# Performance work log

Hardware: AMD Instinct MI355X
Metric: run time of the kernel (lower is better)

Reference implementation:

```python
import jax, jax.numpy as jnp
import numpy as np

DISCARD_RATIOS = [0.25, 1.0, 1.0, 1.0, 0.25, 0.25, 1.0, 1.0, 1.0, 1.0, 0.25, 0.25]
START_LAYER = 4
SKIP_LAYERS = {5, 6, 7, 8, 9, 10}

L, B, H, N = 12, 32, 12, 197


def setup_inputs() -> dict:
    key = jax.random.key(0)
    # post-softmax-like attention weights: positive, uniform in [0,1)
    attentions = jax.random.uniform(key, (L, B, H, N, N), dtype=jnp.float32)
    return {"attentions": attentions}


def reference(attentions) -> jnp.ndarray:
    Ln, Bn, Hn, Nn, _ = attentions.shape
    I = jnp.eye(Nn, dtype=attentions.dtype)            # [N,N]
    result = jnp.broadcast_to(I, (Bn, Nn, Nn))         # [B,N,N]
    b_idx = jnp.arange(Bn)[:, None]                    # [B,1] for batched scatter
    for layer in range(START_LAYER, Ln):
        if layer in SKIP_LAYERS:
            continue
        attn = attentions[layer].mean(axis=1)          # head fusion 'mean' -> [B,N,N]
        k = int(Nn * Nn * DISCARD_RATIOS[layer])       # static per-layer discard count
        if k > 0:
            flat = attn.reshape(Bn, -1)                # [B, N*N]
            # indices of the k SMALLEST entries per batch (torch topk largest=False)
            _, idx = jax.lax.top_k(-flat, k)           # [B,k]
            col0 = flat[:, 0]                          # protect flat index 0 (CLS->CLS)
            flat = flat.at[b_idx, idx].set(0.0)
            flat = flat.at[:, 0].set(col0)
            attn = flat.reshape(Bn, Nn, Nn)
        attn = (attn + I[None]) * 0.5
        attn = attn / attn.sum(axis=-1, keepdims=True)
        result = jnp.einsum('bij,bjk->bik', attn, result)
    return result


if __name__ == "__main__":
    out = reference(**setup_inputs())
    print(out.shape, out.dtype)
```

## Files before the change

### kernel.cpp

```cpp
#include <hip/hip_runtime.h>
#include <stdint.h>

#define Lc   12
#define Bc   32
#define Hc   12
#define Nc   197
#define NNc  (Nc * Nc)
#define Kc   9702
#define NLB  64

#define HBINS 2048
#define CAP   2048

__global__ void __launch_bounds__(256) head_mean_kernel(const float* __restrict__ in,
                                                        float* __restrict__ mean) {
    int j  = blockIdx.x * 256 + threadIdx.x;
    int lb = blockIdx.y;
    if (j >= NNc) return;
    int lsel  = lb >> 5;
    int b     = lb & 31;
    int layer = lsel ? 11 : 4;
    const float* base = in + ((size_t)(layer * Bc + b)) * Hc * NNc + j;
    float acc = 0.0f;
    #pragma unroll
    for (int h = 0; h < Hc; ++h) acc += base[(size_t)h * NNc];
    mean[(size_t)lb * NNc + j] = acc / 12.0f;
}

__global__ void __launch_bounds__(256) select_kernel(const float* __restrict__ mean,
                                                     int* __restrict__ thr_out,
                                                     int* __restrict__ cut_out) {
    const int lb  = blockIdx.x;
    const int tid = threadIdx.x;
    const float* v = mean + (size_t)lb * NNc;

    __shared__ int hist[HBINS];
    __shared__ int chunk[256];
    __shared__ int s_bin, s_cum, s_cnt;
    __shared__ int list[CAP];

    const int shifts[3] = {21, 10, 0};
    const int masks[3]  = {0x7FF, 0x7FF, 0x3FF};

    int kreq = Kc;
    unsigned prefix = 0;

    for (int pass = 0; pass < 3; ++pass) {
        for (int i = tid; i < HBINS; i += 256) hist[i] = 0;
        __syncthreads();
        for (int i = tid; i < NNc; i += 256) {
            unsigned bits = __float_as_uint(v[i]);
            bool ok = (pass == 0) || ((bits >> shifts[pass - 1]) == prefix);
            if (ok) atomicAdd(&hist[(bits >> shifts[pass]) & masks[pass]], 1);
        }
        __syncthreads();
        int s = 0;
        #pragma unroll
        for (int q = 0; q < 8; ++q) s += hist[tid * 8 + q];
        chunk[tid] = s;
        __syncthreads();
        if (tid == 0) {
            int run = 0;
            for (int t = 0; t < 256; ++t) { int tmp = chunk[t]; chunk[t] = run; run += tmp; }
        }
        __syncthreads();
        {
            int c = chunk[tid];
            #pragma unroll
            for (int q = 0; q < 8; ++q) {
                int h = hist[tid * 8 + q];
                if (c < kreq && c + h >= kreq) { s_bin = tid * 8 + q; s_cum = c; }
                c += h;
            }
        }
        __syncthreads();
        kreq -= s_cum;
        if (pass == 0)      prefix = (unsigned)s_bin;
        else if (pass == 1) prefix = (prefix << 11) | (unsigned)s_bin;
        else                prefix = (prefix << 10) | (unsigned)s_bin;
        __syncthreads();
    }

    if (tid == 0) s_cnt = 0;
    __syncthreads();
    for (int i = tid; i < NNc; i += 256) {
        if (__float_as_uint(v[i]) == prefix) {
            int p = atomicAdd(&s_cnt, 1);
            if (p < CAP) list[p] = i;
        }
    }
    __syncthreads();
    if (tid == 0) {
        int m = s_cnt < CAP ? s_cnt : CAP;
        int t = kreq;
        int last = -1;
        for (int s2 = 0; s2 < t && s2 < m; ++s2) {
            int mn = 0x7FFFFFFF;
            for (int q = 0; q < m; ++q) { int x = list[q]; if (x > last && x < mn) mn = x; }
            last = mn;
        }
        thr_out[lb] = (int)prefix;
        cut_out[lb] = last;
    }
}

__global__ void __launch_bounds__(256) norm_kernel(float* __restrict__ buf,
                                                   const int* __restrict__ thr_arr,
                                                   const int* __restrict__ cut_arr) {
    int row = blockIdx.x;
    int lb  = row / Nc;
    int i   = row - lb * Nc;
    float thr  = __uint_as_float((unsigned)thr_arr[lb]);
    int cutoff = cut_arr[lb];
    float* rowp = buf + (size_t)lb * NNc + (size_t)i * Nc;

    int j = threadIdx.x;
    float a = 0.0f;
    if (j < Nc) {
        float vv = rowp[j];
        int idx  = i * Nc + j;
        bool zero = (idx != 0) && (vv < thr || (vv == thr && idx <= cutoff));
        float x = zero ? 0.0f : vv;
        a = (x + (i == j ? 1.0f : 0.0f)) * 0.5f;
    }
    float s = a;
    #pragma unroll
    for (int off = 32; off > 0; off >>= 1) s += __shfl_down(s, off, 64);
    __shared__ float red[4];
    __shared__ float s_tot;
    int wid = threadIdx.x >> 6;
    if ((threadIdx.x & 63) == 0) red[wid] = s;
    __syncthreads();
    if (threadIdx.x == 0) s_tot = red[0] + red[1] + red[2] + red[3];
    __syncthreads();
    if (j < Nc) rowp[j] = a / s_tot;
}

__global__ void __launch_bounds__(256) matmul_kernel(const float* __restrict__ buf,
                                                     float* __restrict__ C) {
    int b  = blockIdx.z;
    const float* A  = buf + (size_t)(32 + b) * NNc;
    const float* Bm = buf + (size_t)b * NNc;
    float* Cb = C + (size_t)b * NNc;

    __shared__ float As[16][17];
    __shared__ float Bs[16][17];
    int tx = threadIdx.x, ty = threadIdx.y;
    int i0 = blockIdx.y * 16, j0 = blockIdx.x * 16;
    float acc = 0.0f;
    for (int k0 = 0; k0 < Nc; k0 += 16) {
        int ar = i0 + ty, ac = k0 + tx;
        As[ty][tx] = (ar < Nc && ac < Nc) ? A[ar * Nc + ac] : 0.0f;
        int br = k0 + ty, bc = j0 + tx;
        Bs[ty][tx] = (br < Nc && bc < Nc) ? Bm[br * Nc + bc] : 0.0f;
        __syncthreads();
        #pragma unroll
        for (int kk = 0; kk < 16; ++kk) acc += As[ty][kk] * Bs[kk][tx];
        __syncthreads();
    }
    int i = i0 + ty, j = j0 + tx;
    if (i < Nc && j < Nc) Cb[i * Nc + j] = acc;
}

extern "C" void kernel_launch(void* const* d_in, const int* in_sizes, int n_in,
                              void* d_out, int out_size, void* d_ws, size_t ws_size,
                              hipStream_t stream) {
    const float* attn = (const float*)d_in[0];
    float* out = (float*)d_out;

    float* buf = (float*)d_ws;
    int*   thr = (int*)((char*)d_ws + (size_t)NLB * NNc * sizeof(float));
    int*   cut = thr + NLB;

    dim3 g1((NNc + 255) / 256, NLB);
    head_mean_kernel<<<g1, 256, 0, stream>>>(attn, buf);

    select_kernel<<<NLB, 256, 0, stream>>>(buf, thr, cut);

    norm_kernel<<<NLB * Nc, 256, 0, stream>>>(buf, thr, cut);

    matmul_kernel<<<dim3(13, 13, Bc), dim3(16, 16), 0, stream>>>(buf, out);
}
```

Before: 928.7 us.

## Vectorize head mean, fuse select with normalization, enlarge matmul tiles

The head-mean kernel now handles four elements per thread into a padded, float4-aligned buffer. The radix-select and row-normalization kernels are merged into a single 1024-thread block per batch-layer, with a wave-level scan replacing the serial prefix sum and float4 loads in the histogram passes. The matmul moves to 32x32 tiles with a 2x2 register block per thread. The fused kernel still runs only 64 blocks, so normalization gets less parallelism than the old per-row launch in exchange for removing a launch and a global round trip.

```diff
diff --git a/kernel.cpp b/kernel.cpp
--- a/kernel.cpp
+++ b/kernel.cpp
@@ -6,74 +6,108 @@
 #define Hc   12
 #define Nc   197
 #define NNc  (Nc * Nc)
+#define NG4  9703
+#define STRIDEc 38812
 #define Kc   9702
 #define NLB  64
 
 #define HBINS 2048
 #define CAP   2048
+#define PADV  2.0f
 
 __global__ void __launch_bounds__(256) head_mean_kernel(const float* __restrict__ in,
                                                         float* __restrict__ mean) {
-    int j  = blockIdx.x * 256 + threadIdx.x;
+    int j4 = blockIdx.x * 256 + threadIdx.x;
     int lb = blockIdx.y;
-    if (j >= NNc) return;
-    int lsel  = lb >> 5;
+    if (j4 >= NG4) return;
     int b     = lb & 31;
-    int layer = lsel ? 11 : 4;
+    int layer = (lb >> 5) ? 11 : 4;
+    int j = j4 * 4;
     const float* base = in + ((size_t)(layer * Bc + b)) * Hc * NNc + j;
-    float acc = 0.0f;
-    #pragma unroll
-    for (int h = 0; h < Hc; ++h) acc += base[(size_t)h * NNc];
-    mean[(size_t)lb * NNc + j] = acc / 12.0f;
-}
-
-__global__ void __launch_bounds__(256) select_kernel(const float* __restrict__ mean,
-                                                     int* __restrict__ thr_out,
-                                                     int* __restrict__ cut_out) {
-    const int lb  = blockIdx.x;
-    const int tid = threadIdx.x;
-    const float* v = mean + (size_t)lb * NNc;
+    float* mp = mean + (size_t)lb * STRIDEc;
+
+    if (j + 4 <= NNc) {
+        float a0 = 0.f, a1 = 0.f, a2 = 0.f, a3 = 0.f;
+        #pragma unroll
+        for (int h = 0; h < Hc; ++h) {
+            const float* p = base + (size_t)h * NNc;
+            a0 += p[0]; a1 += p[1]; a2 += p[2]; a3 += p[3];
+        }
+        float4 r;
+        r.x = a0 / 12.0f; r.y = a1 / 12.0f; r.z = a2 / 12.0f; r.w = a3 / 12.0f;
+        *reinterpret_cast<float4*>(mp + j) = r;
+    } else {
+        for (int e = j; e < STRIDEc; ++e) {
+            if (e < NNc) {
+                float a = 0.f;
+                #pragma unroll
+                for (int h = 0; h < Hc; ++h) a += base[(size_t)h * NNc + (e - j)];
+                mp[e] = a / 12.0f;
+            } else {
+                mp[e] = PADV;
+            }
+        }
+    }
+}
+
+__global__ void __launch_bounds__(1024) select_norm_kernel(float* __restrict__ mean) {
+    const int lb   = blockIdx.x;
+    const int tid  = threadIdx.x;
+    const int lane = tid & 63;
+    const int wid  = tid >> 6;
+    float* vbuf = mean + (size_t)lb * STRIDEc;
+    const float4* v4 = reinterpret_cast<const float4*>(vbuf);
 
     __shared__ int hist[HBINS];
-    __shared__ int chunk[256];
-    __shared__ int s_bin, s_cum, s_cnt;
+    __shared__ int wtot[16];
+    __shared__ int s_bin, s_cum, s_cnt, s_cut;
     __shared__ int list[CAP];
-
-    const int shifts[3] = {21, 10, 0};
-    const int masks[3]  = {0x7FF, 0x7FF, 0x3FF};
 
     int kreq = Kc;
     unsigned prefix = 0;
 
+    #pragma unroll
     for (int pass = 0; pass < 3; ++pass) {
-        for (int i = tid; i < HBINS; i += 256) hist[i] = 0;
-        __syncthreads();
-        for (int i = tid; i < NNc; i += 256) {
-            unsigned bits = __float_as_uint(v[i]);
-            bool ok = (pass == 0) || ((bits >> shifts[pass - 1]) == prefix);
-            if (ok) atomicAdd(&hist[(bits >> shifts[pass]) & masks[pass]], 1);
-        }
-        __syncthreads();
-        int s = 0;
-        #pragma unroll
-        for (int q = 0; q < 8; ++q) s += hist[tid * 8 + q];
-        chunk[tid] = s;
-        __syncthreads();
-        if (tid == 0) {
-            int run = 0;
-            for (int t = 0; t < 256; ++t) { int tmp = chunk[t]; chunk[t] = run; run += tmp; }
-        }
-        __syncthreads();
-        {
-            int c = chunk[tid];
+        const int shift  = (pass == 0) ? 21 : (pass == 1) ? 10 : 0;
+        const int mask   = (pass == 2) ? 0x3FF : 0x7FF;
+        const int pshift = (pass == 1) ? 21 : 10;
+
+        for (int i = tid; i < HBINS; i += 1024) hist[i] = 0;
+        __syncthreads();
+
+        for (int i = tid; i < NG4; i += 1024) {
+            float4 vv = v4[i];
+            float vals[4] = {vv.x, vv.y, vv.z, vv.w};
             #pragma unroll
-            for (int q = 0; q < 8; ++q) {
-                int h = hist[tid * 8 + q];
-                if (c < kreq && c + h >= kreq) { s_bin = tid * 8 + q; s_cum = c; }
-                c += h;
-            }
-        }
-        __syncthreads();
+            for (int c = 0; c < 4; ++c) {
+                unsigned bits = __float_as_uint(vals[c]);
+                bool ok = (pass == 0) || ((bits >> pshift) == prefix);
+                if (ok) atomicAdd(&hist[(bits >> shift) & mask], 1);
+            }
+        }
+        __syncthreads();
+
+        int h0 = hist[2 * tid];
+        int h1 = hist[2 * tid + 1];
+        int pairSum = h0 + h1;
+        int incl = pairSum;
+        #pragma unroll
+        for (int off = 1; off < 64; off <<= 1) {
+            int t = __shfl_up(incl, off, 64);
+            if (lane >= off) incl += t;
+        }
+        if (lane == 63) wtot[wid] = incl;
+        __syncthreads();
+        int woff = 0;
+        #pragma unroll
+        for (int w = 0; w < 16; ++w) woff += (w < wid) ? wtot[w] : 0;
+        int excl = woff + incl - pairSum;
+
+        int c0 = excl, c1 = excl + h0;
+        if (c0 < kreq && c0 + h0 >= kreq) { s_bin = 2 * tid;     s_cum = c0; }
+        if (c1 < kreq && c1 + h1 >= kreq) { s_bin = 2 * tid + 1; s_cum = c1; }
+        __syncthreads();
+
         kreq -= s_cum;
         if (pass == 0)      prefix = (unsigned)s_bin;
         else if (pass == 1) prefix = (prefix << 11) | (unsigned)s_bin;
@@ -83,10 +117,15 @@
 
     if (tid == 0) s_cnt = 0;
     __syncthreads();
-    for (int i = tid; i < NNc; i += 256) {
-        if (__float_as_uint(v[i]) == prefix) {
-            int p = atomicAdd(&s_cnt, 1);
-            if (p < CAP) list[p] = i;
+    for (int i = tid; i < NG4; i += 1024) {
+        float4 vv = v4[i];
+        float vals[4] = {vv.x, vv.y, vv.z, vv.w};
+        #pragma unroll
+        for (int c = 0; c < 4; ++c) {
+            if (__float_as_uint(vals[c]) == prefix) {
+                int p = atomicAdd(&s_cnt, 1);
+                if (p < CAP) list[p] = i * 4 + c;
+            }
         }
     }
     __syncthreads();
@@ -99,67 +138,84 @@
             for (int q = 0; q < m; ++q) { int x = list[q]; if (x > last && x < mn) mn = x; }
             last = mn;
         }
-        thr_out[lb] = (int)prefix;
-        cut_out[lb] = last;
-    }
-}
-
-__global__ void __launch_bounds__(256) norm_kernel(float* __restrict__ buf,
-                                                   const int* __restrict__ thr_arr,
-                                                   const int* __restrict__ cut_arr) {
-    int row = blockIdx.x;
-    int lb  = row / Nc;
-    int i   = row - lb * Nc;
-    float thr  = __uint_as_float((unsigned)thr_arr[lb]);
-    int cutoff = cut_arr[lb];
-    float* rowp = buf + (size_t)lb * NNc + (size_t)i * Nc;
-
-    int j = threadIdx.x;
-    float a = 0.0f;
-    if (j < Nc) {
-        float vv = rowp[j];
-        int idx  = i * Nc + j;
-        bool zero = (idx != 0) && (vv < thr || (vv == thr && idx <= cutoff));
-        float x = zero ? 0.0f : vv;
-        a = (x + (i == j ? 1.0f : 0.0f)) * 0.5f;
-    }
-    float s = a;
-    #pragma unroll
-    for (int off = 32; off > 0; off >>= 1) s += __shfl_down(s, off, 64);
-    __shared__ float red[4];
-    __shared__ float s_tot;
-    int wid = threadIdx.x >> 6;
-    if ((threadIdx.x & 63) == 0) red[wid] = s;
+        s_cut = last;
+    }
     __syncthreads();
-    if (threadIdx.x == 0) s_tot = red[0] + red[1] + red[2] + red[3];
-    __syncthreads();
-    if (j < Nc) rowp[j] = a / s_tot;
+
+    const float thr = __uint_as_float(prefix);
+    const int   cut = s_cut;
+
+    for (int r = wid; r < Nc; r += 16) {
+        float a[4];
+        float sum = 0.f;
+        #pragma unroll
+        for (int q = 0; q < 4; ++q) {
+            int c = lane + q * 64;
+            float av = 0.f;
+            if (c < Nc) {
+                int idx  = r * Nc + c;
+                float vv = vbuf[idx];
+                bool zero = (idx != 0) && (vv < thr || (vv == thr && idx <= cut));
+                float x = zero ? 0.f : vv;
+                av = (x + (r == c ? 1.0f : 0.0f)) * 0.5f;
+            }
+            a[q] = av;
+            sum += av;
+        }
+        #pragma unroll
+        for (int off = 32; off > 0; off >>= 1) sum += __shfl_xor(sum, off, 64);
+        #pragma unroll
+        for (int q = 0; q < 4; ++q) {
+            int c = lane + q * 64;
+            if (c < Nc) vbuf[r * Nc + c] = a[q] / sum;
+        }
+    }
 }
 
 __global__ void __launch_bounds__(256) matmul_kernel(const float* __restrict__ buf,
                                                      float* __restrict__ C) {
-    int b  = blockIdx.z;
-    const float* A  = buf + (size_t)(32 + b) * NNc;
-    const float* Bm = buf + (size_t)b * NNc;
+    int b = blockIdx.z;
+    const float* A  = buf + (size_t)(32 + b) * STRIDEc;
+    const float* Bm = buf + (size_t)b * STRIDEc;
     float* Cb = C + (size_t)b * NNc;
 
-    __shared__ float As[16][17];
-    __shared__ float Bs[16][17];
-    int tx = threadIdx.x, ty = threadIdx.y;
-    int i0 = blockIdx.y * 16, j0 = blockIdx.x * 16;
-    float acc = 0.0f;
-    for (int k0 = 0; k0 < Nc; k0 += 16) {
-        int ar = i0 + ty, ac = k0 + tx;
-        As[ty][tx] = (ar < Nc && ac < Nc) ? A[ar * Nc + ac] : 0.0f;
-        int br = k0 + ty, bc = j0 + tx;
-        Bs[ty][tx] = (br < Nc && bc < Nc) ? Bm[br * Nc + bc] : 0.0f;
-        __syncthreads();
-        #pragma unroll
-        for (int kk = 0; kk < 16; ++kk) acc += As[ty][kk] * Bs[kk][tx];
-        __syncthreads();
-    }
+    __shared__ float As[32][33];
+    __shared__ float Bs[32][33];
+    int tid = threadIdx.x;
+    int tx = tid & 15, ty = tid >> 4;
+    int i0 = blockIdx.y * 32, j0 = blockIdx.x * 32;
+    float acc00 = 0.f, acc01 = 0.f, acc10 = 0.f, acc11 = 0.f;
+
+    for (int k0 = 0; k0 < Nc; k0 += 32) {
+        #pragma unroll
+        for (int q = 0; q < 4; ++q) {
+            int e = tid + q * 256;
+            int r = e >> 5, c2 = e & 31;
+            int ar = i0 + r, ac = k0 + c2;
+            As[r][c2] = (ar < Nc && ac < Nc) ? A[ar * Nc + ac] : 0.f;
+            int br = k0 + r, bc = j0 + c2;
+            Bs[r][c2] = (br < Nc && bc < Nc) ? Bm[br * Nc + bc] : 0.f;
+        }
+        __syncthreads();
+        #pragma unroll
+        for (int kk = 0; kk < 32; ++kk) {
+            float a0 = As[ty][kk],      a1 = As[ty + 16][kk];
+            float b0 = Bs[kk][tx],      b1 = Bs[kk][tx + 16];
+            acc00 += a0 * b0; acc01 += a0 * b1;
+            acc10 += a1 * b0; acc11 += a1 * b1;
+        }
+        __syncthreads();
+    }
+
     int i = i0 + ty, j = j0 + tx;
-    if (i < Nc && j < Nc) Cb[i * Nc + j] = acc;
+    if (i < Nc) {
+        if (j < Nc)      Cb[i * Nc + j]        = acc00;
+        if (j + 16 < Nc) Cb[i * Nc + j + 16]   = acc01;
+    }
+    if (i + 16 < Nc) {
+        if (j < Nc)      Cb[(i + 16) * Nc + j]      = acc10;
+        if (j + 16 < Nc) Cb[(i + 16) * Nc + j + 16] = acc11;
+    }
 }
 
 extern "C" void kernel_launch(void* const* d_in, const int* in_sizes, int n_in,
@@ -169,15 +225,11 @@
     float* out = (float*)d_out;
 
     float* buf = (float*)d_ws;
-    int*   thr = (int*)((char*)d_ws + (size_t)NLB * NNc * sizeof(float));
-    int*   cut = thr + NLB;
-
-    dim3 g1((NNc + 255) / 256, NLB);
+
+    dim3 g1((NG4 + 255) / 256, NLB);
     head_mean_kernel<<<g1, 256, 0, stream>>>(attn, buf);
 
-    select_kernel<<<NLB, 256, 0, stream>>>(buf, thr, cut);
-
-    norm_kernel<<<NLB * Nc, 256, 0, stream>>>(buf, thr, cut);
-
-    matmul_kernel<<<dim3(13, 13, Bc), dim3(16, 16), 0, stream>>>(buf, out);
-}
+    select_norm_kernel<<<NLB, 1024, 0, stream>>>(buf);
+
+    matmul_kernel<<<dim3(7, 7, Bc), dim3(256), 0, stream>>>(buf, out);
+}
```

Result: faster. 845.1 us (-9.0%).
